# Kernel optimization log

Measured on AMD Instinct MI355X. Metric: run time of the kernel, lower is better.

Reference implementation:

```python
import jax, jax.numpy as jnp
import numpy as np


def setup_inputs() -> dict:
    key = jax.random.key(0)
    k1, k2 = jax.random.split(key)
    x = jax.random.normal(k1, (16, 8192, 128), dtype=jnp.float32)
    embed = jax.random.normal(k2, (1024, 128), dtype=jnp.float32)
    return {"x": x, "embed": embed}


def reference(x, embed):
    # preprocess: flatten leading dims -> (N, d)
    shape = x.shape
    xf = x.reshape(-1, shape[-1])  # (N, d)
    # quantize: negative squared Euclidean distance, argmax over codebook
    dist = (2.0 * (xf @ embed.T)
            - jnp.sum(xf * xf, axis=1, keepdims=True)
            - jnp.sum(embed * embed, axis=1)[None, :])
    embed_ind = jnp.argmax(dist, axis=-1)  # (N,)
    # postprocess indices back to input leading shape
    embed_ind = embed_ind.reshape(shape[:-1])
    # dequantize: embedding lookup
    quantize = embed[embed_ind]  # (..., d)
    return embed_ind, quantize
```

## Files before the change

kernel.cpp:

```cpp
#include <hip/hip_runtime.h>
#include <math.h>


typedef __attribute__((ext_vector_type(8)))  short short8_t;
typedef __attribute__((ext_vector_type(16))) float floatx16;

constexpr int D        = 128;
constexpr int KCODES   = 1024;
constexpr int NTILES   = 32;
constexpr int ROWS_BLK = 128;
constexpr float TAU    = 0.015f;
constexpr unsigned LIST_CAP = 65536;

constexpr size_t WS_COUNTER = 0;
constexpr size_t WS_CSQ     = 256;
constexpr size_t WS_EHI     = 8192;
constexpr size_t WS_ELO     = WS_EHI + 262144;
constexpr size_t WS_LIST    = WS_ELO + 262144;
constexpr size_t WS_EMBT    = WS_LIST + 262144;

#define GLOBAL_AS __attribute__((address_space(1)))
#define LDS_AS    __attribute__((address_space(3)))

__device__ inline unsigned short bf16_rne(float v, float* back) {
    unsigned u = __float_as_uint(v);
    unsigned r = (u + 0x7FFFu + ((u >> 16) & 1u)) >> 16;
    *back = __uint_as_float(r << 16);
    return (unsigned short)r;
}

__global__ void ecb_prep(const float* __restrict__ embed, float* __restrict__ csq,
                         unsigned short* __restrict__ ehi, unsigned short* __restrict__ elo,
                         float* __restrict__ embT, unsigned int* __restrict__ counter) {
    int n = blockIdx.x * 64 + threadIdx.x;
    if (n == 0) *counter = 0u;
    if (n >= KCODES) return;
    const int t = n >> 5, nn = n & 31, nm = nn & 15;
    const float* row = embed + (size_t)n * D;
    const size_t tb = (size_t)t * 32 * D + (size_t)nn * D;
    float s = 0.f;
#pragma unroll
    for (int cc = 0; cc < 16; ++cc) {
        float4 a  = *(const float4*)(row + cc * 8);
        float4 bq = *(const float4*)(row + cc * 8 + 4);
        s = fmaf(a.x, a.x, s);  s = fmaf(a.y, a.y, s);
        s = fmaf(a.z, a.z, s);  s = fmaf(a.w, a.w, s);
        s = fmaf(bq.x, bq.x, s); s = fmaf(bq.y, bq.y, s);
        s = fmaf(bq.z, bq.z, s); s = fmaf(bq.w, bq.w, s);
        float vv[8] = {a.x, a.y, a.z, a.w, bq.x, bq.y, bq.z, bq.w};
#pragma unroll
        for (int j = 0; j < 8; ++j) embT[(size_t)(cc * 8 + j) * KCODES + n] = vv[j];
        unsigned short h[8], l[8];
#pragma unroll
        for (int j = 0; j < 8; ++j) {
            float hb, db;
            h[j] = bf16_rne(vv[j], &hb);
            l[j] = bf16_rne(vv[j] - hb, &db);
        }
        uint4 ph, pl;
        ph.x = (unsigned)h[0] | ((unsigned)h[1] << 16);
        ph.y = (unsigned)h[2] | ((unsigned)h[3] << 16);
        ph.z = (unsigned)h[4] | ((unsigned)h[5] << 16);
        ph.w = (unsigned)h[6] | ((unsigned)h[7] << 16);
        pl.x = (unsigned)l[0] | ((unsigned)l[1] << 16);
        pl.y = (unsigned)l[2] | ((unsigned)l[3] << 16);
        pl.z = (unsigned)l[4] | ((unsigned)l[5] << 16);
        pl.w = (unsigned)l[6] | ((unsigned)l[7] << 16);
        size_t dst = tb + (size_t)((cc ^ nm) * 8);
        *(uint4*)(ehi + dst) = ph;
        *(uint4*)(elo + dst) = pl;
    }
    csq[n] = s;
}

__global__ __launch_bounds__(256, 3)
void ecb_main(const float* __restrict__ x,
              const unsigned short* __restrict__ ehi, const unsigned short* __restrict__ elo,
              const float* __restrict__ csq, const float* __restrict__ embed,
              float* __restrict__ out_idx, float* __restrict__ out_q,
              unsigned int* __restrict__ counter, unsigned int* __restrict__ list) {
    __shared__ unsigned short ebuf[2][2][4096];
    __shared__ int sidx[ROWS_BLK];

    const int tid  = threadIdx.x;
    const int lane = tid & 63, wave = tid >> 6;
    const int col  = lane & 31, h = lane >> 5, colm = col & 15;
    const long rowblk = (long)blockIdx.x * ROWS_BLK;
    const int  roww   = wave * 32;

    short8_t ah[8], al[8];
    {
        const float* xr = x + (rowblk + roww + col) * (long)D + h * 8;
#pragma unroll
        for (int c = 0; c < 8; ++c) {
            float4 a  = *(const float4*)(xr + c * 16);
            float4 bq = *(const float4*)(xr + c * 16 + 4);
            float vv[8] = {a.x, a.y, a.z, a.w, bq.x, bq.y, bq.z, bq.w};
            short8_t fh, fl;
#pragma unroll
            for (int j = 0; j < 8; ++j) {
                float hb, db;
                fh[j] = (short)bf16_rne(vv[j], &hb);
                fl[j] = (short)bf16_rne(vv[j] - hb, &db);
            }
            ah[c] = fh;
            al[c] = fl;
        }
    }

    auto stage = [&](int t, int b) {
        const char* gh = (const char*)(ehi) + (size_t)t * 8192;
        const char* gl = (const char*)(elo) + (size_t)t * 8192;
        char* lh = (char*)&ebuf[b][0][0];
        char* ll = (char*)&ebuf[b][1][0];
#pragma unroll
        for (int i = 0; i < 2; ++i) {
            int off = i * 4096 + wave * 1024;
            __builtin_amdgcn_global_load_lds((const GLOBAL_AS unsigned int*)(gh + off + lane * 16),
                                             (LDS_AS unsigned int*)(lh + off), 16, 0, 0);
            __builtin_amdgcn_global_load_lds((const GLOBAL_AS unsigned int*)(gl + off + lane * 16),
                                             (LDS_AS unsigned int*)(ll + off), 16, 0, 0);
        }
    };

    float v1[16], v2[16];
#pragma unroll
    for (int j = 0; j < 16; ++j) { v1[j] = -INFINITY; v2[j] = -INFINITY; }

    stage(0, 0);
    __syncthreads();

#pragma unroll 1
    for (int t = 0; t < NTILES; ++t) {
        const int b = t & 1;
        if (t + 1 < NTILES) stage(t + 1, (t + 1) & 1);

        const float cs = csq[t * 32 + col];

        floatx16 accA, accB;
#pragma unroll
        for (int i = 0; i < 16; ++i) { accA[i] = 0.f; accB[i] = 0.f; }

#pragma unroll
        for (int s = 0; s < 8; ++s) {
            const int cc = 2 * s + h;
            const int idx = (col * 16 + (cc ^ colm)) * 8;
            short8_t bh = *(const short8_t*)&ebuf[b][0][idx];
            short8_t bl = *(const short8_t*)&ebuf[b][1][idx];
            accA = __builtin_amdgcn_mfma_f32_32x32x16_bf16(ah[s], bh, accA, 0, 0, 0);
            accB = __builtin_amdgcn_mfma_f32_32x32x16_bf16(al[s], bh, accB, 0, 0, 0);
            accB = __builtin_amdgcn_mfma_f32_32x32x16_bf16(ah[s], bl, accB, 0, 0, 0);
        }

#pragma unroll
        for (int j = 0; j < 16; ++j) {
            float sc = fmaf(2.f, accA[j] + accB[j], -cs);
            unsigned u = (__float_as_uint(sc) & ~31u) | (unsigned)t;
            float cand = __uint_as_float(u);
            float mn = fminf(v1[j], cand);
            v1[j] = fmaxf(v1[j], cand);
            v2[j] = fmaxf(v2[j], mn);
        }
        __syncthreads();
    }

#pragma unroll
    for (int j = 0; j < 16; ++j) {
        float a1 = v1[j], a2 = v2[j];
        int   c1 = ((__float_as_uint(a1) & 31u) << 5) | col;
#pragma unroll
        for (int m = 1; m < 32; m <<= 1) {
            float o1 = __shfl_xor(a1, m, 64);
            int   oc = __shfl_xor(c1, m, 64);
            float o2 = __shfl_xor(a2, m, 64);
            float lo = fminf(a1, o1);
            if (o1 > a1) { a1 = o1; c1 = oc; }
            a2 = fmaxf(fmaxf(a2, o2), lo);
        }
        if (col == j) {
            int row_local = roww + (j & 3) + 8 * (j >> 2) + 4 * h;
            long grow = rowblk + row_local;
            sidx[row_local] = c1;
            out_idx[grow] = (float)c1;
            if (a1 - a2 < TAU) {
                unsigned p = atomicAdd(counter, 1u);
                if (p < LIST_CAP) list[p] = (unsigned)grow;
            }
        }
    }
    __syncthreads();

    for (int i = tid; i < ROWS_BLK * 32; i += 256) {
        int r = i >> 5, q = i & 31;
        int code = sidx[r];
        float4 v = *(const float4*)(embed + (size_t)code * D + q * 4);
        *(float4*)(out_q + (rowblk + r) * (long)D + q * 4) = v;
    }
}

__global__ __launch_bounds__(256)
void ecb_recheck(const float* __restrict__ x, const float* __restrict__ embT,
                 const float* __restrict__ embed, const float* __restrict__ csq,
                 float* __restrict__ out_idx, float* __restrict__ out_q,
                 const unsigned int* __restrict__ counter,
                 const unsigned int* __restrict__ list) {
    __shared__ float xs[D];
    __shared__ float bv[256];
    __shared__ int   bi[256];
    const int tid = threadIdx.x;
    unsigned cnt = *counter;
    if (cnt > LIST_CAP) cnt = LIST_CAP;
    const float4* eT = (const float4*)embT;

    for (unsigned it = blockIdx.x; it < cnt; it += gridDim.x) {
        const long row = (long)list[it];
        if (tid < 32) *(float4*)&xs[tid * 4] = *(const float4*)(x + row * D + tid * 4);
        __syncthreads();

        float4 dot = {0.f, 0.f, 0.f, 0.f};
        for (int k = 0; k < D; ++k) {
            float xv = xs[k];
            float4 e = eT[(size_t)k * 256 + tid];
            dot.x = fmaf(xv, e.x, dot.x);
            dot.y = fmaf(xv, e.y, dot.y);
            dot.z = fmaf(xv, e.z, dot.z);
            dot.w = fmaf(xv, e.w, dot.w);
        }
        const int c0 = tid * 4;
        float best = -INFINITY; int bidx = 0;
        float scs[4] = {fmaf(2.f, dot.x, -csq[c0]),
                        fmaf(2.f, dot.y, -csq[c0 + 1]),
                        fmaf(2.f, dot.z, -csq[c0 + 2]),
                        fmaf(2.f, dot.w, -csq[c0 + 3])};
#pragma unroll
        for (int i = 0; i < 4; ++i)
            if (scs[i] > best) { best = scs[i]; bidx = c0 + i; }
        bv[tid] = best; bi[tid] = bidx;
        __syncthreads();
        for (int s = 128; s > 0; s >>= 1) {
            if (tid < s) {
                float ov = bv[tid + s]; int oi = bi[tid + s];
                if (ov > bv[tid] || (ov == bv[tid] && oi < bi[tid])) { bv[tid] = ov; bi[tid] = oi; }
            }
            __syncthreads();
        }
        const int win = bi[0];
        if (tid == 0) out_idx[row] = (float)win;
        if (tid < 32) {
            float4 v = *(const float4*)(embed + (size_t)win * D + tid * 4);
            *(float4*)(out_q + row * D + tid * 4) = v;
        }
        __syncthreads();
    }
}

extern "C" void kernel_launch(void* const* d_in, const int* in_sizes, int n_in,
                              void* d_out, int out_size, void* d_ws, size_t ws_size,
                              hipStream_t stream) {
    const float* x     = (const float*)d_in[0];
    const float* embed = (const float*)d_in[1];
    const int N = in_sizes[0] / D;
    char* ws = (char*)d_ws;
    unsigned int*   counter = (unsigned int*)(ws + WS_COUNTER);
    float*          csq     = (float*)(ws + WS_CSQ);
    unsigned short* ehi     = (unsigned short*)(ws + WS_EHI);
    unsigned short* elo     = (unsigned short*)(ws + WS_ELO);
    unsigned int*   list    = (unsigned int*)(ws + WS_LIST);
    float*          embT    = (float*)(ws + WS_EMBT);
    float* out_idx = (float*)d_out;
    float* out_q   = out_idx + N;

    hipLaunchKernelGGL(ecb_prep, dim3(16), dim3(64), 0, stream,
                       embed, csq, ehi, elo, embT, counter);
    hipLaunchKernelGGL(ecb_main, dim3(N / ROWS_BLK), dim3(256), 0, stream,
                       x, ehi, elo, csq, embed, out_idx, out_q, counter, list);
    hipLaunchKernelGGL(ecb_recheck, dim3(1024), dim3(256), 0, stream,
                       x, embT, embed, csq, out_idx, out_q, counter, list);
}
```

Measured before the change: 235.5 us.

## Fuse near-tie recheck into main kernel with per-block LDS list

Removes the separate recheck kernel and global atomic list. Each block now collects its ambiguous rows in an LDS list and re-scores them exactly in fp32 after writing its outputs. Also folds the factor 2 into the bf16-split x operands, seeds the accumulator with the negated code norms, uses fmed3 for second-best tracking, and issues the first tile stage before converting x. This saves a kernel launch and global atomics, but blocks with many near-ties now serialize that exact work inside the main kernel, and doubling x before the bf16 split can shift rounding slightly.

```diff
diff --git a/kernel.cpp b/kernel.cpp
--- a/kernel.cpp
+++ b/kernel.cpp
@@ -10,14 +10,11 @@
 constexpr int NTILES   = 32;
 constexpr int ROWS_BLK = 128;
 constexpr float TAU    = 0.015f;
-constexpr unsigned LIST_CAP = 65536;
-
-constexpr size_t WS_COUNTER = 0;
-constexpr size_t WS_CSQ     = 256;
-constexpr size_t WS_EHI     = 8192;
-constexpr size_t WS_ELO     = WS_EHI + 262144;
-constexpr size_t WS_LIST    = WS_ELO + 262144;
-constexpr size_t WS_EMBT    = WS_LIST + 262144;
+
+constexpr size_t WS_NCSQ = 0;
+constexpr size_t WS_EHI  = 4096;
+constexpr size_t WS_ELO  = WS_EHI + 262144;
+constexpr size_t WS_EMBT = WS_ELO + 262144;
 
 #define GLOBAL_AS __attribute__((address_space(1)))
 #define LDS_AS    __attribute__((address_space(3)))
@@ -29,11 +26,10 @@
     return (unsigned short)r;
 }
 
-__global__ void ecb_prep(const float* __restrict__ embed, float* __restrict__ csq,
+__global__ void ecb_prep(const float* __restrict__ embed, float* __restrict__ ncsq,
                          unsigned short* __restrict__ ehi, unsigned short* __restrict__ elo,
-                         float* __restrict__ embT, unsigned int* __restrict__ counter) {
+                         float* __restrict__ embT) {
     int n = blockIdx.x * 64 + threadIdx.x;
-    if (n == 0) *counter = 0u;
     if (n >= KCODES) return;
     const int t = n >> 5, nn = n & 31, nm = nn & 15;
     const float* row = embed + (size_t)n * D;
@@ -70,17 +66,19 @@
         *(uint4*)(ehi + dst) = ph;
         *(uint4*)(elo + dst) = pl;
     }
-    csq[n] = s;
+    ncsq[n] = -s;
 }
 
 __global__ __launch_bounds__(256, 3)
 void ecb_main(const float* __restrict__ x,
               const unsigned short* __restrict__ ehi, const unsigned short* __restrict__ elo,
-              const float* __restrict__ csq, const float* __restrict__ embed,
-              float* __restrict__ out_idx, float* __restrict__ out_q,
-              unsigned int* __restrict__ counter, unsigned int* __restrict__ list) {
+              const float* __restrict__ ncsq, const float* __restrict__ embed,
+              const float* __restrict__ embT,
+              float* __restrict__ out_idx, float* __restrict__ out_q) {
     __shared__ unsigned short ebuf[2][2][4096];
     __shared__ int sidx[ROWS_BLK];
+    __shared__ unsigned char llist[ROWS_BLK];
+    __shared__ unsigned lcount;
 
     const int tid  = threadIdx.x;
     const int lane = tid & 63, wave = tid >> 6;
@@ -88,25 +86,7 @@
     const long rowblk = (long)blockIdx.x * ROWS_BLK;
     const int  roww   = wave * 32;
 
-    short8_t ah[8], al[8];
-    {
-        const float* xr = x + (rowblk + roww + col) * (long)D + h * 8;
-#pragma unroll
-        for (int c = 0; c < 8; ++c) {
-            float4 a  = *(const float4*)(xr + c * 16);
-            float4 bq = *(const float4*)(xr + c * 16 + 4);
-            float vv[8] = {a.x, a.y, a.z, a.w, bq.x, bq.y, bq.z, bq.w};
-            short8_t fh, fl;
-#pragma unroll
-            for (int j = 0; j < 8; ++j) {
-                float hb, db;
-                fh[j] = (short)bf16_rne(vv[j], &hb);
-                fl[j] = (short)bf16_rne(vv[j] - hb, &db);
-            }
-            ah[c] = fh;
-            al[c] = fl;
-        }
-    }
+    if (tid == 0) lcount = 0u;
 
     auto stage = [&](int t, int b) {
         const char* gh = (const char*)(ehi) + (size_t)t * 8192;
@@ -123,11 +103,33 @@
         }
     };
 
+    stage(0, 0);
+
+    short8_t ah[8], al[8];
+    {
+        const float* xr = x + (rowblk + roww + col) * (long)D + h * 8;
+#pragma unroll
+        for (int c = 0; c < 8; ++c) {
+            float4 a  = *(const float4*)(xr + c * 16);
+            float4 bq = *(const float4*)(xr + c * 16 + 4);
+            float vv[8] = {a.x, a.y, a.z, a.w, bq.x, bq.y, bq.z, bq.w};
+            short8_t fh, fl;
+#pragma unroll
+            for (int j = 0; j < 8; ++j) {
+                float v2x = vv[j] + vv[j];
+                float hb, db;
+                fh[j] = (short)bf16_rne(v2x, &hb);
+                fl[j] = (short)bf16_rne(v2x - hb, &db);
+            }
+            ah[c] = fh;
+            al[c] = fl;
+        }
+    }
+
     float v1[16], v2[16];
 #pragma unroll
     for (int j = 0; j < 16; ++j) { v1[j] = -INFINITY; v2[j] = -INFINITY; }
 
-    stage(0, 0);
     __syncthreads();
 
 #pragma unroll 1
@@ -135,11 +137,11 @@
         const int b = t & 1;
         if (t + 1 < NTILES) stage(t + 1, (t + 1) & 1);
 
-        const float cs = csq[t * 32 + col];
+        const float negcs = ncsq[t * 32 + col];
 
         floatx16 accA, accB;
 #pragma unroll
-        for (int i = 0; i < 16; ++i) { accA[i] = 0.f; accB[i] = 0.f; }
+        for (int i = 0; i < 16; ++i) { accA[i] = negcs; accB[i] = 0.f; }
 
 #pragma unroll
         for (int s = 0; s < 8; ++s) {
@@ -154,12 +156,12 @@
 
 #pragma unroll
         for (int j = 0; j < 16; ++j) {
-            float sc = fmaf(2.f, accA[j] + accB[j], -cs);
+            float sc = accA[j] + accB[j];
             unsigned u = (__float_as_uint(sc) & ~31u) | (unsigned)t;
             float cand = __uint_as_float(u);
-            float mn = fminf(v1[j], cand);
-            v1[j] = fmaxf(v1[j], cand);
-            v2[j] = fmaxf(v2[j], mn);
+            float vo = v1[j];
+            v1[j] = fmaxf(vo, cand);
+            v2[j] = __builtin_amdgcn_fmed3f(vo, v2[j], cand);
         }
         __syncthreads();
     }
@@ -167,7 +169,7 @@
 #pragma unroll
     for (int j = 0; j < 16; ++j) {
         float a1 = v1[j], a2 = v2[j];
-        int   c1 = ((__float_as_uint(a1) & 31u) << 5) | col;
+        int   c1 = (int)((__float_as_uint(a1) & 31u) << 5) | col;
 #pragma unroll
         for (int m = 1; m < 32; m <<= 1) {
             float o1 = __shfl_xor(a1, m, 64);
@@ -179,12 +181,11 @@
         }
         if (col == j) {
             int row_local = roww + (j & 3) + 8 * (j >> 2) + 4 * h;
-            long grow = rowblk + row_local;
             sidx[row_local] = c1;
-            out_idx[grow] = (float)c1;
+            out_idx[rowblk + row_local] = (float)c1;
             if (a1 - a2 < TAU) {
-                unsigned p = atomicAdd(counter, 1u);
-                if (p < LIST_CAP) list[p] = (unsigned)grow;
+                unsigned p = atomicAdd(&lcount, 1u);
+                llist[p] = (unsigned char)row_local;
             }
         }
     }
@@ -193,31 +194,23 @@
     for (int i = tid; i < ROWS_BLK * 32; i += 256) {
         int r = i >> 5, q = i & 31;
         int code = sidx[r];
-        float4 v = *(const float4*)(embed + (size_t)code * D + q * 4);
-        *(float4*)(out_q + (rowblk + r) * (long)D + q * 4) = v;
-    }
-}
-
-__global__ __launch_bounds__(256)
-void ecb_recheck(const float* __restrict__ x, const float* __restrict__ embT,
-                 const float* __restrict__ embed, const float* __restrict__ csq,
-                 float* __restrict__ out_idx, float* __restrict__ out_q,
-                 const unsigned int* __restrict__ counter,
-                 const unsigned int* __restrict__ list) {
-    __shared__ float xs[D];
-    __shared__ float bv[256];
-    __shared__ int   bi[256];
-    const int tid = threadIdx.x;
-    unsigned cnt = *counter;
-    if (cnt > LIST_CAP) cnt = LIST_CAP;
+        float4 ev = *(const float4*)(embed + (size_t)code * D + q * 4);
+        *(float4*)(out_q + (rowblk + r) * (long)D + q * 4) = ev;
+    }
+    __syncthreads();
+
+    float* xs = (float*)&ebuf[0][0][0];
+    float* bv = xs + D;
+    int*   bi = (int*)(bv + 256);
+    const unsigned nf = lcount;
     const float4* eT = (const float4*)embT;
-
-    for (unsigned it = blockIdx.x; it < cnt; it += gridDim.x) {
-        const long row = (long)list[it];
+    for (unsigned f = 0; f < nf; ++f) {
+        const int rl  = llist[f];
+        const long row = rowblk + rl;
         if (tid < 32) *(float4*)&xs[tid * 4] = *(const float4*)(x + row * D + tid * 4);
         __syncthreads();
-
         float4 dot = {0.f, 0.f, 0.f, 0.f};
+#pragma unroll 8
         for (int k = 0; k < D; ++k) {
             float xv = xs[k];
             float4 e = eT[(size_t)k * 256 + tid];
@@ -227,11 +220,12 @@
             dot.w = fmaf(xv, e.w, dot.w);
         }
         const int c0 = tid * 4;
+        float4 nc = *(const float4*)(ncsq + c0);
+        float scs[4] = {fmaf(2.f, dot.x, nc.x),
+                        fmaf(2.f, dot.y, nc.y),
+                        fmaf(2.f, dot.z, nc.z),
+                        fmaf(2.f, dot.w, nc.w)};
         float best = -INFINITY; int bidx = 0;
-        float scs[4] = {fmaf(2.f, dot.x, -csq[c0]),
-                        fmaf(2.f, dot.y, -csq[c0 + 1]),
-                        fmaf(2.f, dot.z, -csq[c0 + 2]),
-                        fmaf(2.f, dot.w, -csq[c0 + 3])};
 #pragma unroll
         for (int i = 0; i < 4; ++i)
             if (scs[i] > best) { best = scs[i]; bidx = c0 + i; }
@@ -247,8 +241,8 @@
         const int win = bi[0];
         if (tid == 0) out_idx[row] = (float)win;
         if (tid < 32) {
-            float4 v = *(const float4*)(embed + (size_t)win * D + tid * 4);
-            *(float4*)(out_q + row * D + tid * 4) = v;
+            float4 ev = *(const float4*)(embed + (size_t)win * D + tid * 4);
+            *(float4*)(out_q + row * D + tid * 4) = ev;
         }
         __syncthreads();
     }
@@ -261,19 +255,15 @@
     const float* embed = (const float*)d_in[1];
     const int N = in_sizes[0] / D;
     char* ws = (char*)d_ws;
-    unsigned int*   counter = (unsigned int*)(ws + WS_COUNTER);
-    float*          csq     = (float*)(ws + WS_CSQ);
-    unsigned short* ehi     = (unsigned short*)(ws + WS_EHI);
-    unsigned short* elo     = (unsigned short*)(ws + WS_ELO);
-    unsigned int*   list    = (unsigned int*)(ws + WS_LIST);
-    float*          embT    = (float*)(ws + WS_EMBT);
+    float*          ncsq = (float*)(ws + WS_NCSQ);
+    unsigned short* ehi  = (unsigned short*)(ws + WS_EHI);
+    unsigned short* elo  = (unsigned short*)(ws + WS_ELO);
+    float*          embT = (float*)(ws + WS_EMBT);
     float* out_idx = (float*)d_out;
     float* out_q   = out_idx + N;
 
     hipLaunchKernelGGL(ecb_prep, dim3(16), dim3(64), 0, stream,
-                       embed, csq, ehi, elo, embT, counter);
+                       embed, ncsq, ehi, elo, embT);
     hipLaunchKernelGGL(ecb_main, dim3(N / ROWS_BLK), dim3(256), 0, stream,
-                       x, ehi, elo, csq, embed, out_idx, out_q, counter, list);
-    hipLaunchKernelGGL(ecb_recheck, dim3(1024), dim3(256), 0, stream,
-                       x, embT, embed, csq, out_idx, out_q, counter, list);
-}
+                       x, ehi, elo, ncsq, embed, embT, out_idx, out_q);
+}
```

After: 239.2 us. About the same (+1.6%).
